# Performance work log

Measured on AMD Instinct MI355X. Metric: run time of the kernel, lower is better.

Reference implementation:

```python
import jax, jax.numpy as jnp
import numpy as np

K = 16  # kNN neighbors (global k in the original source)
# channel progression of the 6 DynamicEdgeConv layers
DIMS = [3, 32, 128, 256, 64, 32, 16]


def _knn_idx(x, k):
    # x: [B, N, D] -> indices of k nearest neighbors (incl. self), [B, N, k]
    sq = jnp.sum(x * x, axis=-1)                                   # [B, N]
    d = sq[:, :, None] + sq[:, None, :] - 2.0 * jnp.einsum('bnd,bmd->bnm', x, x)
    _, idx = jax.lax.top_k(-d, k)                                  # smallest distances
    return idx


def _edge_conv(x, W1, b1, W2, b2, k):
    # DynamicEdgeConv with mean aggregation: message = MLP([x_i, x_j - x_i])
    idx = _knn_idx(x, k)                                           # [B, N, k]
    xj = jax.vmap(lambda xb, ib: xb[ib])(x, idx)                   # [B, N, k, D]
    xi = jnp.broadcast_to(x[:, :, None, :], xj.shape)
    e = jnp.concatenate([xi, xj - xi], axis=-1)                    # [B, N, k, 2D]
    h = jax.nn.relu(e @ W1 + b1)
    h = jax.nn.relu(h @ W2 + b2)
    return jnp.mean(h, axis=2)                                     # [B, N, d_out]


def setup_inputs() -> dict:
    key = jax.random.key(0)
    ks = jax.random.split(key, 32)
    inp = {'x': jax.random.normal(ks[0], (8, 2048, 3), dtype=jnp.float32)}
    for l in range(6):
        din, dout = DIMS[l], DIMS[l + 1]
        s1 = 1.0 / np.sqrt(2 * din)
        s2 = 1.0 / np.sqrt(2 * dout)
        inp[f'W1_{l}'] = jax.random.normal(ks[1 + 4 * l], (2 * din, 2 * dout), dtype=jnp.float32) * s1
        inp[f'b1_{l}'] = jnp.zeros((2 * dout,), dtype=jnp.float32)
        inp[f'W2_{l}'] = jax.random.normal(ks[2 + 4 * l], (2 * dout, dout), dtype=jnp.float32) * s2
        inp[f'b2_{l}'] = jnp.zeros((dout,), dtype=jnp.float32)
    inp['Wf'] = jax.random.normal(ks[30], (16, 2), dtype=jnp.float32) * 0.25
    inp['bf'] = jnp.zeros((2,), dtype=jnp.float32)
    return inp


def reference(x, W1_0, b1_0, W2_0, b2_0, W1_1, b1_1, W2_1, b2_1,
              W1_2, b1_2, W2_2, b2_2, W1_3, b1_3, W2_3, b2_3,
              W1_4, b1_4, W2_4, b2_4, W1_5, b1_5, W2_5, b2_5, Wf, bf):
    params = [(W1_0, b1_0, W2_0, b2_0), (W1_1, b1_1, W2_1, b2_1),
              (W1_2, b1_2, W2_2, b2_2), (W1_3, b1_3, W2_3, b2_3),
              (W1_4, b1_4, W2_4, b2_4), (W1_5, b1_5, W2_5, b2_5)]
    for (W1, b1, W2, b2) in params:
        x = _edge_conv(x, W1, b1, W2, b2, K)
        x = jax.nn.relu(x)  # extra ReLU from forward (dropout is eval-mode identity)
    pooled = jnp.mean(x, axis=1)        # global_mean_pool over nodes -> [B, 16]
    return pooled @ Wf + bf             # [B, 2]
```

## Files before the change

kernel.cpp:

```cpp
#include <hip/hip_runtime.h>
#include <math.h>

#define NPTS 2048
#define NB 8
#define BN 16384
#define KNN 16

typedef _Float16 half4 __attribute__((ext_vector_type(4)));
typedef _Float16 half8 __attribute__((ext_vector_type(8)));
typedef float floatx16 __attribute__((ext_vector_type(16)));

__global__ __launch_bounds__(256) void sqprep_kernel(const float* __restrict__ X,
                                                     float* __restrict__ SQ,
                                                     const float* __restrict__ W1,
                                                     const float* __restrict__ b1,
                                                     float* __restrict__ Wcat,
                                                     float* __restrict__ bcat,
                                                     int din, int d2,
                                                     const float* __restrict__ W2,
                                                     _Float16* __restrict__ W2H,
                                                     _Float16* __restrict__ W2L,
                                                     int dout, int pb) {
    const int bid = blockIdx.x;
    if (bid < BN / 256) {
        int g = bid * 256 + threadIdx.x;
        const float* row = X + (size_t)g * din;
        float s = 0.f;
        for (int d = 0; d < din; ++d) s = fmaf(row[d], row[d], s);
        SQ[g] = s;
    } else if (bid < BN / 256 + pb) {
        int n4 = 2 * d2;
        int total = din * n4;
        int i = (bid - BN / 256) * 256 + threadIdx.x;
        if (i < total) {
            int d = i / n4, c = i - d * n4;
            float v;
            if (c < d2) v = W1[d * d2 + c] - W1[(din + d) * d2 + c];
            else        v = W1[(din + d) * d2 + (c - d2)];
            Wcat[i] = v;
        }
        if (i < n4) bcat[i] = (i < d2) ? b1[i] : 0.f;
    } else {
        int i = (bid - BN / 256 - pb) * 256 + threadIdx.x;
        if (i < d2 * dout) {
            int k = i / dout, c = i - k * dout;
            float wv = W2[i];
            _Float16 hv = (_Float16)wv;
            float rv = wv - (float)hv;
            W2H[(size_t)c * d2 + k] = hv;
            W2L[(size_t)c * d2 + k] = (_Float16)rv;
        }
    }
}

template <int DIN>
__global__ __launch_bounds__(256) void gram_kernel(const float* __restrict__ X,
                                                   const float* __restrict__ SQ,
                                                   float* __restrict__ DT) {
    __shared__ float As[32][132];
    __shared__ float Bs[32][132];
    const int t = threadIdx.x;
    const int tx = t & 15, ty = t >> 4;
    int bid = blockIdx.x;
    int bi = 0;
    while (bid >= 16 - bi) { bid -= 16 - bi; ++bi; }
    const int bj = bi + bid;
    const int i0 = bi * 128;
    const int j0 = bj * 128;
    const int z = blockIdx.z;
    const float* Xb = X + (size_t)z * NPTS * DIN;
    const float* SQb = SQ + (size_t)z * NPTS;
    float* DTb = DT + (size_t)z * NPTS * NPTS;

    const int e = t & 127;

    float acc[8][8];
    #pragma unroll
    for (int i = 0; i < 8; ++i)
        #pragma unroll
        for (int j = 0; j < 8; ++j) acc[i][j] = 0.f;

    if constexpr (DIN % 32 == 0) {
        const int rh = (t >> 7) * 16;
        const float* Ar = Xb + (size_t)(i0 + e) * DIN;
        const float* Br = Xb + (size_t)(j0 + e) * DIN;
        for (int k0 = 0; k0 < DIN; k0 += 32) {
            #pragma unroll
            for (int h = 0; h < 4; ++h) {
                float4 a = *(const float4*)(Ar + k0 + rh + h * 4);
                float4 b = *(const float4*)(Br + k0 + rh + h * 4);
                As[rh + h * 4 + 0][e] = a.x; As[rh + h * 4 + 1][e] = a.y;
                As[rh + h * 4 + 2][e] = a.z; As[rh + h * 4 + 3][e] = a.w;
                Bs[rh + h * 4 + 0][e] = b.x; Bs[rh + h * 4 + 1][e] = b.y;
                Bs[rh + h * 4 + 2][e] = b.z; Bs[rh + h * 4 + 3][e] = b.w;
            }
            __syncthreads();
            #pragma unroll
            for (int r = 0; r < 32; ++r) {
                float4 a0 = *(const float4*)&As[r][ty * 4];
                float4 a1 = *(const float4*)&As[r][64 + ty * 4];
                float4 b0 = *(const float4*)&Bs[r][tx * 4];
                float4 b1 = *(const float4*)&Bs[r][64 + tx * 4];
                float av[8] = {a0.x, a0.y, a0.z, a0.w, a1.x, a1.y, a1.z, a1.w};
                float bv[8] = {b0.x, b0.y, b0.z, b0.w, b1.x, b1.y, b1.z, b1.w};
                #pragma unroll
                for (int i = 0; i < 8; ++i)
                    #pragma unroll
                    for (int j = 0; j < 8; ++j)
                        acc[i][j] = fmaf(av[i], bv[j], acc[i][j]);
            }
            __syncthreads();
        }
    } else {
        const int rh = (t >> 7) * 8;
        #pragma unroll
        for (int i = 0; i < 8; ++i) {
            int k = rh + i;
            As[rh + i][e] = (k < DIN) ? Xb[(size_t)(i0 + e) * DIN + k] : 0.f;
            Bs[rh + i][e] = (k < DIN) ? Xb[(size_t)(j0 + e) * DIN + k] : 0.f;
        }
        __syncthreads();
        #pragma unroll
        for (int r = 0; r < 16; ++r) {
            float4 a0 = *(const float4*)&As[r][ty * 4];
            float4 a1 = *(const float4*)&As[r][64 + ty * 4];
            float4 b0 = *(const float4*)&Bs[r][tx * 4];
            float4 b1 = *(const float4*)&Bs[r][64 + tx * 4];
            float av[8] = {a0.x, a0.y, a0.z, a0.w, a1.x, a1.y, a1.z, a1.w};
            float bv[8] = {b0.x, b0.y, b0.z, b0.w, b1.x, b1.y, b1.z, b1.w};
            #pragma unroll
            for (int i = 0; i < 8; ++i)
                #pragma unroll
                for (int j = 0; j < 8; ++j)
                    acc[i][j] = fmaf(av[i], bv[j], acc[i][j]);
        }
        __syncthreads();
    }

    float sqi[8], sqj[8];
    #pragma unroll
    for (int i = 0; i < 8; ++i) {
        int ro = (i < 4) ? (ty * 4 + i) : (64 + ty * 4 + (i - 4));
        sqi[i] = SQb[i0 + ro];
    }
    #pragma unroll
    for (int j = 0; j < 8; ++j) {
        int co = (j < 4) ? (tx * 4 + j) : (64 + tx * 4 + (j - 4));
        sqj[j] = SQb[j0 + co];
    }
    #pragma unroll
    for (int i = 0; i < 8; ++i) {
        int ro = (i < 4) ? (ty * 4 + i) : (64 + ty * 4 + (i - 4));
        float* out = DTb + (size_t)(i0 + ro) * NPTS + j0;
        float4 o0, o1;
        o0.x = (sqi[i] + sqj[0]) - 2.f * acc[i][0];
        o0.y = (sqi[i] + sqj[1]) - 2.f * acc[i][1];
        o0.z = (sqi[i] + sqj[2]) - 2.f * acc[i][2];
        o0.w = (sqi[i] + sqj[3]) - 2.f * acc[i][3];
        o1.x = (sqi[i] + sqj[4]) - 2.f * acc[i][4];
        o1.y = (sqi[i] + sqj[5]) - 2.f * acc[i][5];
        o1.z = (sqi[i] + sqj[6]) - 2.f * acc[i][6];
        o1.w = (sqi[i] + sqj[7]) - 2.f * acc[i][7];
        *(float4*)(out + tx * 4) = o0;
        *(float4*)(out + 64 + tx * 4) = o1;
    }
    if (bi != bj) {
        #pragma unroll
        for (int j = 0; j < 8; ++j) {
            int co = (j < 4) ? (tx * 4 + j) : (64 + tx * 4 + (j - 4));
            float* out = DTb + (size_t)(j0 + co) * NPTS + i0;
            float4 o0, o1;
            o0.x = (sqi[0] + sqj[j]) - 2.f * acc[0][j];
            o0.y = (sqi[1] + sqj[j]) - 2.f * acc[1][j];
            o0.z = (sqi[2] + sqj[j]) - 2.f * acc[2][j];
            o0.w = (sqi[3] + sqj[j]) - 2.f * acc[3][j];
            o1.x = (sqi[4] + sqj[j]) - 2.f * acc[4][j];
            o1.y = (sqi[5] + sqj[j]) - 2.f * acc[5][j];
            o1.z = (sqi[6] + sqj[j]) - 2.f * acc[6][j];
            o1.w = (sqi[7] + sqj[j]) - 2.f * acc[7][j];
            *(float4*)(out + ty * 4) = o0;
            *(float4*)(out + 64 + ty * 4) = o1;
        }
    }
}

__global__ __launch_bounds__(256) void knn_select_kernel(const float* __restrict__ DT,
                                                         int* __restrict__ IDX, int qoff) {
    const int t = threadIdx.x;
    const int w = t >> 6, lane = t & 63;
    const int q = blockIdx.x * 4 + w;
    const float* dq = DT + (size_t)q * NPTS;
    const int l4 = lane << 2;

    float vals[32];
    #pragma unroll
    for (int s = 0; s < 8; ++s) {
        float4 v = *(const float4*)(dq + s * 256 + l4);
        vals[s * 4 + 0] = v.x; vals[s * 4 + 1] = v.y;
        vals[s * 4 + 2] = v.z; vals[s * 4 + 3] = v.w;
    }
    unsigned rm = 0;
    float best = INFINITY; int bslot = 32;
    #pragma unroll
    for (int sl = 0; sl < 32; ++sl)
        if (vals[sl] < best) { best = vals[sl]; bslot = sl; }

    for (int rep = 0; rep < KNN; ++rep) {
        int bj = (bslot < 32) ? ((bslot >> 2) * 256 + l4 + (bslot & 3)) : NPTS;
        float gb = best; int gj = bj;
        #pragma unroll
        for (int off = 1; off < 64; off <<= 1) {
            float ov = __shfl_xor(gb, off);
            int oj = __shfl_xor(gj, off);
            if (ov < gb || (ov == gb && oj < gj)) { gb = ov; gj = oj; }
        }
        if (lane == 0) IDX[(size_t)(qoff + q) * KNN + rep] = gj;
        if (((gj >> 2) & 63) == lane) {
            int slot = ((gj >> 8) << 2) | (gj & 3);
            rm |= (1u << slot);
            best = INFINITY; bslot = 32;
            #pragma unroll
            for (int sl = 0; sl < 32; ++sl)
                if (!(rm & (1u << sl)) && vals[sl] < best) { best = vals[sl]; bslot = sl; }
        }
    }
}

template <int KK, int NN>
__global__ __launch_bounds__(256) void gemm_big_kernel(const float* __restrict__ A,
                                                       const float* __restrict__ B,
                                                       const float* __restrict__ bias,
                                                       float* __restrict__ C) {
    __shared__ float As[32][132];
    __shared__ float Bs[32][132];
    const int t = threadIdx.x;
    const int tx = t & 15, ty = t >> 4;
    const int m0 = blockIdx.x * 128;
    const int c0 = blockIdx.y * 128;

    float acc[8][8];
    #pragma unroll
    for (int i = 0; i < 8; ++i)
        #pragma unroll
        for (int j = 0; j < 8; ++j) acc[i][j] = 0.f;

    const int e = t & 127;
    const int rh = (t >> 7) * 16;
    const float* Ar = A + (size_t)(m0 + e) * KK + rh;
    const int br = t & 31;
    const int bc = (t >> 5) * 16;
    const float* Wbase = B + (size_t)br * NN + c0 + bc;

    for (int k0 = 0; k0 < KK; k0 += 32) {
        #pragma unroll
        for (int h = 0; h < 4; ++h) {
            float4 a = *(const float4*)(Ar + k0 + h * 4);
            As[rh + h * 4 + 0][e] = a.x; As[rh + h * 4 + 1][e] = a.y;
            As[rh + h * 4 + 2][e] = a.z; As[rh + h * 4 + 3][e] = a.w;
            *(float4*)&Bs[br][bc + h * 4] = *(const float4*)(Wbase + (size_t)k0 * NN + h * 4);
        }
        __syncthreads();
        #pragma unroll
        for (int r = 0; r < 32; ++r) {
            float4 a0 = *(const float4*)&As[r][ty * 4];
            float4 a1 = *(const float4*)&As[r][64 + ty * 4];
            float4 b0 = *(const float4*)&Bs[r][tx * 4];
            float4 b1 = *(const float4*)&Bs[r][64 + tx * 4];
            float av[8] = {a0.x, a0.y, a0.z, a0.w, a1.x, a1.y, a1.z, a1.w};
            float bv[8] = {b0.x, b0.y, b0.z, b0.w, b1.x, b1.y, b1.z, b1.w};
            #pragma unroll
            for (int i = 0; i < 8; ++i)
                #pragma unroll
                for (int j = 0; j < 8; ++j)
                    acc[i][j] = fmaf(av[i], bv[j], acc[i][j]);
        }
        __syncthreads();
    }

    float bvv[8];
    #pragma unroll
    for (int j = 0; j < 8; ++j) {
        int co = (j < 4) ? (tx * 4 + j) : (64 + tx * 4 + (j - 4));
        bvv[j] = bias[c0 + co];
    }
    #pragma unroll
    for (int i = 0; i < 8; ++i) {
        int ro = (i < 4) ? (ty * 4 + i) : (64 + ty * 4 + (i - 4));
        float* out = C + (size_t)(m0 + ro) * NN + c0;
        float4 o0, o1;
        o0.x = acc[i][0] + bvv[0]; o0.y = acc[i][1] + bvv[1];
        o0.z = acc[i][2] + bvv[2]; o0.w = acc[i][3] + bvv[3];
        o1.x = acc[i][4] + bvv[4]; o1.y = acc[i][5] + bvv[5];
        o1.z = acc[i][6] + bvv[6]; o1.w = acc[i][7] + bvv[7];
        *(float4*)(out + tx * 4) = o0;
        *(float4*)(out + 64 + tx * 4) = o1;
    }
}

template <int KK, int NN>
__global__ __launch_bounds__(256) void gemm_pq_kernel(const float* __restrict__ A,
                                                      const float* __restrict__ B,
                                                      const float* __restrict__ bias,
                                                      float* __restrict__ C) {
    __shared__ float As[16][68];
    __shared__ float Bs[16][64];
    const int t = threadIdx.x;
    const int tx = t & 15, ty = t >> 4;
    const int m0 = blockIdx.x * 64;
    const int c0 = blockIdx.y * 64;
    float acc[4][4];
    #pragma unroll
    for (int i = 0; i < 4; ++i)
        #pragma unroll
        for (int j = 0; j < 4; ++j) acc[i][j] = 0.f;

    constexpr int KCH = (KK + 15) / 16;
    for (int kc = 0; kc < KCH; ++kc) {
        const int k0 = kc * 16;
        {
            int m = t & 63;
            int r4 = (t >> 6) * 4;
            if constexpr (KK % 16 == 0) {
                float4 v = *(const float4*)(A + (size_t)(m0 + m) * KK + k0 + r4);
                As[r4 + 0][m] = v.x; As[r4 + 1][m] = v.y;
                As[r4 + 2][m] = v.z; As[r4 + 3][m] = v.w;
            } else {
                #pragma unroll
                for (int i = 0; i < 4; ++i) {
                    int r = r4 + i;
                    As[r][m] = (k0 + r < KK) ? A[(size_t)(m0 + m) * KK + k0 + r] : 0.f;
                }
            }
        }
        {
            int r = t >> 4;
            int c = (t & 15) * 4;
            float4 v = make_float4(0.f, 0.f, 0.f, 0.f);
            if (k0 + r < KK) v = *(const float4*)(B + (size_t)(k0 + r) * NN + c0 + c);
            *(float4*)&Bs[r][c] = v;
        }
        __syncthreads();
        #pragma unroll
        for (int r = 0; r < 16; ++r) {
            float4 a4 = *(const float4*)&As[r][ty * 4];
            float4 b4 = *(const float4*)&Bs[r][tx * 4];
            float av[4] = {a4.x, a4.y, a4.z, a4.w};
            float bv[4] = {b4.x, b4.y, b4.z, b4.w};
            #pragma unroll
            for (int i = 0; i < 4; ++i)
                #pragma unroll
                for (int j = 0; j < 4; ++j)
                    acc[i][j] = fmaf(av[i], bv[j], acc[i][j]);
        }
        __syncthreads();
    }
    float4 bv4 = *(const float4*)(bias + c0 + tx * 4);
    float bv[4] = {bv4.x, bv4.y, bv4.z, bv4.w};
    #pragma unroll
    for (int i = 0; i < 4; ++i) {
        float4 o;
        o.x = acc[i][0] + bv[0];
        o.y = acc[i][1] + bv[1];
        o.z = acc[i][2] + bv[2];
        o.w = acc[i][3] + bv[3];
        *(float4*)(C + (size_t)(m0 + ty * 4 + i) * NN + c0 + tx * 4) = o;
    }
}

template <int D2, int DOUT>
__global__ __launch_bounds__(256) void edge_kernel(const float* __restrict__ PQ,
                                                   const int* __restrict__ IDX,
                                                   const float* __restrict__ W2,
                                                   const float* __restrict__ b2,
                                                   float* __restrict__ Xn) {
    constexpr int N4 = 2 * D2;
    __shared__ float As[16][68];
    __shared__ float Bs[16][64];
    __shared__ int gjs[64];
    const int t = threadIdx.x;
    const int tx = t & 15, ty = t >> 4;
    const int nb = blockIdx.x * 4;
    const int c0 = blockIdx.y * 64;

    if (t < 64) {
        int node = nb + (t >> 4);
        int bstart = (node / NPTS) * NPTS;
        gjs[t] = bstart + IDX[(size_t)node * KNN + (t & 15)];
    }
    __syncthreads();

    float acc[4][4];
    #pragma unroll
    for (int i = 0; i < 4; ++i)
        #pragma unroll
        for (int j = 0; j < 4; ++j) acc[i][j] = 0.f;

    const int e = t & 63;
    const int r4 = (t >> 6) * 4;
    const int gi = nb + (e >> 4);

    for (int k0 = 0; k0 < D2; k0 += 16) {
        {
            int gj = gjs[e];
            float4 p = *(const float4*)(PQ + (size_t)gi * N4 + k0 + r4);
            float4 q = *(const float4*)(PQ + (size_t)gj * N4 + D2 + k0 + r4);
            As[r4 + 0][e] = fmaxf(p.x + q.x, 0.f);
            As[r4 + 1][e] = fmaxf(p.y + q.y, 0.f);
            As[r4 + 2][e] = fmaxf(p.z + q.z, 0.f);
            As[r4 + 3][e] = fmaxf(p.w + q.w, 0.f);
        }
        {
            int r = t >> 4;
            int c = (t & 15) * 4;
            float4 v = make_float4(0.f, 0.f, 0.f, 0.f);
            if (c0 + c < DOUT) v = *(const float4*)(W2 + (size_t)(k0 + r) * DOUT + c0 + c);
            *(float4*)&Bs[r][c] = v;
        }
        __syncthreads();
        #pragma unroll
        for (int r = 0; r < 16; ++r) {
            float4 a4 = *(const float4*)&As[r][ty * 4];
            float4 b4 = *(const float4*)&Bs[r][tx * 4];
            float av[4] = {a4.x, a4.y, a4.z, a4.w};
            float bv[4] = {b4.x, b4.y, b4.z, b4.w};
            #pragma unroll
            for (int i = 0; i < 4; ++i)
                #pragma unroll
                for (int j = 0; j < 4; ++j)
                    acc[i][j] = fmaf(av[i], bv[j], acc[i][j]);
        }
        __syncthreads();
    }

    float bv[4];
    #pragma unroll
    for (int j = 0; j < 4; ++j) {
        int c = c0 + tx * 4 + j;
        bv[j] = (c < DOUT) ? b2[c] : 0.f;
    }
    float s[4];
    #pragma unroll
    for (int j = 0; j < 4; ++j) {
        float ss = 0.f;
        #pragma unroll
        for (int i = 0; i < 4; ++i) ss += fmaxf(acc[i][j] + bv[j], 0.f);
        s[j] = ss;
    }
    #pragma unroll
    for (int j = 0; j < 4; ++j) Bs[ty][tx * 4 + j] = s[j];
    __syncthreads();
    if ((ty & 3) == 0) {
        int node = nb + (ty >> 2);
        #pragma unroll
        for (int j = 0; j < 4; ++j) {
            int c = c0 + tx * 4 + j;
            if (c < DOUT) {
                int cc = tx * 4 + j;
                float tot = Bs[ty][cc] + Bs[ty + 1][cc] + Bs[ty + 2][cc] + Bs[ty + 3][cc];
                Xn[(size_t)node * DOUT + c] = tot * (1.f / 16.f);
            }
        }
    }
}

#define EB_STAGE_MFMA(KC, QQ, POK, KP)                                               \
  {                                                                                  \
    half8 wh0 = *(const half8*)(WHrow + (KC) + rh);                                  \
    half8 wh1 = *(const half8*)(WHrow + (KC) + rh + 8);                              \
    half8 wl0 = *(const half8*)(WLrow + (KC) + rh);                                  \
    half8 wl1 = *(const half8*)(WLrow + (KC) + rh + 8);                              \
    _Pragma("unroll")                                                                \
    for (int h = 0; h < 4; ++h) {                                                    \
      float4 p = *(const float4*)(Prow + (KC) + rh + h * 4);                         \
      float a0 = fmaxf(p.x + QQ[h].x, 0.f);                                          \
      float a1 = fmaxf(p.y + QQ[h].y, 0.f);                                          \
      float a2 = fmaxf(p.z + QQ[h].z, 0.f);                                          \
      float a3 = fmaxf(p.w + QQ[h].w, 0.f);                                          \
      _Float16 h0 = (_Float16)a0, h1 = (_Float16)a1;                                 \
      _Float16 h2 = (_Float16)a2, h3 = (_Float16)a3;                                 \
      half4 hv, lv;                                                                  \
      hv.x = h0; hv.y = h1; hv.z = h2; hv.w = h3;                                    \
      lv.x = (_Float16)(a0 - (float)h0);                                             \
      lv.y = (_Float16)(a1 - (float)h1);                                             \
      lv.z = (_Float16)(a2 - (float)h2);                                             \
      lv.w = (_Float16)(a3 - (float)h3);                                             \
      *(half4*)&Ah[e][rh + h * 4] = hv;                                              \
      *(half4*)&Al[e][rh + h * 4] = lv;                                              \
    }                                                                                \
    *(half8*)&Bh[e][rh] = wh0;                                                       \
    *(half8*)&Bh[e][rh + 8] = wh1;                                                   \
    *(half8*)&Bl[e][rh] = wl0;                                                       \
    *(half8*)&Bl[e][rh + 8] = wl1;                                                   \
    if (POK) {                                                                       \
      _Pragma("unroll")                                                              \
      for (int h = 0; h < 4; ++h)                                                    \
        QQ[h] = *(const float4*)(Qrow + (KP) + rh + h * 4);                          \
    }                                                                                \
    asm volatile("s_waitcnt lgkmcnt(0)" ::: "memory");                               \
    __builtin_amdgcn_s_barrier();                                                    \
    asm volatile("" ::: "memory");                                                   \
    _Pragma("unroll")                                                                \
    for (int ks = 0; ks < 2; ++ks) {                                                 \
      const int kb = ks * 16 + lk;                                                   \
      half8 bf0 = *(const half8*)&Bh[wc + lr][kb];                                   \
      half8 blf0 = *(const half8*)&Bl[wc + lr][kb];                                  \
      half8 bf1 = *(const half8*)&Bh[wc + 32 + lr][kb];                              \
      half8 blf1 = *(const half8*)&Bl[wc + 32 + lr][kb];                             \
      _Pragma("unroll")                                                              \
      for (int i = 0; i < 2; ++i) {                                                  \
        half8 af = *(const half8*)&Ah[wr + i * 32 + lr][kb];                         \
        half8 alf = *(const half8*)&Al[wr + i * 32 + lr][kb];                        \
        acc[i][0] = __builtin_amdgcn_mfma_f32_32x32x16_f16(af, bf0, acc[i][0], 0, 0, 0);   \
        acc[i][0] = __builtin_amdgcn_mfma_f32_32x32x16_f16(af, blf0, acc[i][0], 0, 0, 0);  \
        acc[i][0] = __builtin_amdgcn_mfma_f32_32x32x16_f16(alf, bf0, acc[i][0], 0, 0, 0);  \
        acc[i][1] = __builtin_amdgcn_mfma_f32_32x32x16_f16(af, bf1, acc[i][1], 0, 0, 0);   \
        acc[i][1] = __builtin_amdgcn_mfma_f32_32x32x16_f16(af, blf1, acc[i][1], 0, 0, 0);  \
        acc[i][1] = __builtin_amdgcn_mfma_f32_32x32x16_f16(alf, bf1, acc[i][1], 0, 0, 0);  \
      }                                                                              \
    }                                                                                \
    asm volatile("" ::: "memory");                                                   \
    __builtin_amdgcn_s_barrier();                                                    \
    asm volatile("" ::: "memory");                                                   \
  }

template <int D2, int DOUT>
__global__ __launch_bounds__(256) void edge_big_mfma_kernel(const float* __restrict__ PQ,
                                                            const int* __restrict__ IDX,
                                                            const _Float16* __restrict__ W2H,
                                                            const _Float16* __restrict__ W2L,
                                                            const float* __restrict__ b2,
                                                            float* __restrict__ Xn) {
    constexpr int N4 = 2 * D2;
    __shared__ _Float16 Ah[128][40];
    __shared__ _Float16 Al[128][40];
    __shared__ _Float16 Bh[128][40];
    __shared__ _Float16 Bl[128][40];
    __shared__ int gjs[128];
    const int t = threadIdx.x;
    const int nb8 = blockIdx.x * 8;
    const int c0 = blockIdx.y * 128;

    if (t < 128) {
        int node = nb8 + (t >> 4);
        int bstart = (node / NPTS) * NPTS;
        gjs[t] = bstart + IDX[(size_t)node * KNN + (t & 15)];
    }
    __syncthreads();

    const int e = t & 127;
    const int rh = (t >> 7) * 16;
    const int gi = nb8 + (e >> 4);
    const int gj = gjs[e];
    const float* Prow = PQ + (size_t)gi * N4;
    const float* Qrow = PQ + (size_t)gj * N4 + D2;
    const _Float16* WHrow = W2H + (size_t)(c0 + e) * D2;
    const _Float16* WLrow = W2L + (size_t)(c0 + e) * D2;

    const int w = t >> 6;
    const int lane = t & 63;
    const int wr = (w >> 1) * 64;
    const int wc = (w & 1) * 64;
    const int lr = lane & 31;
    const int lk = (lane >> 5) * 8;
    const int hsel = lane >> 5;

    floatx16 acc[2][2];
    #pragma unroll
    for (int i = 0; i < 2; ++i)
        #pragma unroll
        for (int j = 0; j < 2; ++j)
            #pragma unroll
            for (int r = 0; r < 16; ++r) acc[i][j][r] = 0.f;

    float4 qqA[4], qqB[4];
    #pragma unroll
    for (int h = 0; h < 4; ++h) qqA[h] = *(const float4*)(Qrow + rh + h * 4);
    #pragma unroll
    for (int h = 0; h < 4; ++h) qqB[h] = *(const float4*)(Qrow + 32 + rh + h * 4);

    for (int k0 = 0; k0 < D2; k0 += 64) {
        EB_STAGE_MFMA(k0,      qqA, (k0 + 64 < D2), k0 + 64)
        EB_STAGE_MFMA(k0 + 32, qqB, (k0 + 96 < D2), k0 + 96)
    }

    float bb[2];
    bb[0] = b2[c0 + wc + lr];
    bb[1] = b2[c0 + wc + 32 + lr];
    #pragma unroll
    for (int i = 0; i < 2; ++i) {
        int node0 = nb8 + ((wr + i * 32) >> 4);
        #pragma unroll
        for (int j = 0; j < 2; ++j) {
            float sA = 0.f, sB = 0.f;
            #pragma unroll
            for (int r = 0; r < 8; ++r)  sA += fmaxf(acc[i][j][r] + bb[j], 0.f);
            #pragma unroll
            for (int r = 8; r < 16; ++r) sB += fmaxf(acc[i][j][r] + bb[j], 0.f);
            sA += __shfl_xor(sA, 32);
            sB += __shfl_xor(sB, 32);
            if (hsel == 0) {
                int col = c0 + wc + j * 32 + lr;
                Xn[(size_t)node0 * DOUT + col] = sA * (1.f / 16.f);
                Xn[(size_t)(node0 + 1) * DOUT + col] = sB * (1.f / 16.f);
            }
        }
    }
}
#undef EB_STAGE_MFMA

#define EM_STAGE_MFMA(KC, QQ, POK, KP)                                               \
  {                                                                                  \
    half8 wh0 = *(const half8*)(WHrow + (KC));                                       \
    half8 wl0 = *(const half8*)(WLrow + (KC));                                       \
    _Pragma("unroll")                                                                \
    for (int h = 0; h < 4; ++h) {                                                    \
      float4 p = *(const float4*)(Prow + (KC) + rh + h * 4);                         \
      float a0 = fmaxf(p.x + QQ[h].x, 0.f);                                          \
      float a1 = fmaxf(p.y + QQ[h].y, 0.f);                                          \
      float a2 = fmaxf(p.z + QQ[h].z, 0.f);                                          \
      float a3 = fmaxf(p.w + QQ[h].w, 0.f);                                          \
      _Float16 h0 = (_Float16)a0, h1 = (_Float16)a1;                                 \
      _Float16 h2 = (_Float16)a2, h3 = (_Float16)a3;                                 \
      half4 hv, lv;                                                                  \
      hv.x = h0; hv.y = h1; hv.z = h2; hv.w = h3;                                    \
      lv.x = (_Float16)(a0 - (float)h0);                                             \
      lv.y = (_Float16)(a1 - (float)h1);                                             \
      lv.z = (_Float16)(a2 - (float)h2);                                             \
      lv.w = (_Float16)(a3 - (float)h3);                                             \
      *(half4*)&Ah[e][rh + h * 4] = hv;                                              \
      *(half4*)&Al[e][rh + h * 4] = lv;                                              \
    }                                                                                \
    *(half8*)&Bh[wrB][wkB] = wh0;                                                    \
    *(half8*)&Bl[wrB][wkB] = wl0;                                                    \
    if (POK) {                                                                       \
      _Pragma("unroll")                                                              \
      for (int h = 0; h < 4; ++h)                                                    \
        QQ[h] = *(const float4*)(Qrow + (KP) + rh + h * 4);                          \
    }                                                                                \
    asm volatile("s_waitcnt lgkmcnt(0)" ::: "memory");                               \
    __builtin_amdgcn_s_barrier();                                                    \
    asm volatile("" ::: "memory");                                                   \
    _Pragma("unroll")                                                                \
    for (int ks = 0; ks < 2; ++ks) {                                                 \
      const int kb = ks * 16 + lk;                                                   \
      half8 bf0 = *(const half8*)&Bh[wc + lr][kb];                                   \
      half8 blf0 = *(const half8*)&Bl[wc + lr][kb];                                  \
      _Pragma("unroll")                                                              \
      for (int i = 0; i < 2; ++i) {                                                  \
        half8 af = *(const half8*)&Ah[wr + i * 32 + lr][kb];                         \
        half8 alf = *(const half8*)&Al[wr + i * 32 + lr][kb];                        \
        acc[i] = __builtin_amdgcn_mfma_f32_32x32x16_f16(af, bf0, acc[i], 0, 0, 0);   \
        acc[i] = __builtin_amdgcn_mfma_f32_32x32x16_f16(af, blf0, acc[i], 0, 0, 0);  \
        acc[i] = __builtin_amdgcn_mfma_f32_32x32x16_f16(alf, bf0, acc[i], 0, 0, 0);  \
      }                                                                              \
    }                                                                                \
    asm volatile("" ::: "memory");                                                   \
    __builtin_amdgcn_s_barrier();                                                    \
    asm volatile("" ::: "memory");                                                   \
  }

template <int D2, int DOUT>
__global__ __launch_bounds__(256) void edge_mid_mfma_kernel(const float* __restrict__ PQ,
                                                            const int* __restrict__ IDX,
                                                            const _Float16* __restrict__ W2H,
                                                            const _Float16* __restrict__ W2L,
                                                            const float* __restrict__ b2,
                                                            float* __restrict__ Xn) {
    constexpr int N4 = 2 * D2;
    __shared__ _Float16 Ah[128][40];
    __shared__ _Float16 Al[128][40];
    __shared__ _Float16 Bh[64][40];
    __shared__ _Float16 Bl[64][40];
    __shared__ int gjs[128];
    const int t = threadIdx.x;
    const int nb8 = blockIdx.x * 8;

    if (t < 128) {
        int node = nb8 + (t >> 4);
        int bstart = (node / NPTS) * NPTS;
        gjs[t] = bstart + IDX[(size_t)node * KNN + (t & 15)];
    }
    __syncthreads();

    const int e = t & 127;
    const int rh = (t >> 7) * 16;
    const int gi = nb8 + (e >> 4);
    const int gj = gjs[e];
    const float* Prow = PQ + (size_t)gi * N4;
    const float* Qrow = PQ + (size_t)gj * N4 + D2;
    const int wrB = t & 63;
    const int wkB = (t >> 6) * 8;
    const _Float16* WHrow = W2H + (size_t)wrB * D2 + wkB;
    const _Float16* WLrow = W2L + (size_t)wrB * D2 + wkB;

    const int w = t >> 6;
    const int lane = t & 63;
    const int wr = (w >> 1) * 64;
    const int wc = (w & 1) * 32;
    const int lr = lane & 31;
    const int lk = (lane >> 5) * 8;
    const int hsel = lane >> 5;

    floatx16 acc[2];
    #pragma unroll
    for (int i = 0; i < 2; ++i)
        #pragma unroll
        for (int r = 0; r < 16; ++r) acc[i][r] = 0.f;

    float4 qqA[4], qqB[4];
    #pragma unroll
    for (int h = 0; h < 4; ++h) qqA[h] = *(const float4*)(Qrow + rh + h * 4);
    #pragma unroll
    for (int h = 0; h < 4; ++h) qqB[h] = *(const float4*)(Qrow + 32 + rh + h * 4);

    for (int k0 = 0; k0 < D2; k0 += 64) {
        EM_STAGE_MFMA(k0,      qqA, (k0 + 64 < D2), k0 + 64)
        EM_STAGE_MFMA(k0 + 32, qqB, (k0 + 96 < D2), k0 + 96)
    }

    float bb = b2[wc + lr];
    #pragma unroll
    for (int i = 0; i < 2; ++i) {
        int node0 = nb8 + ((wr + i * 32) >> 4);
        float sA = 0.f, sB = 0.f;
        #pragma unroll
        for (int r = 0; r < 8; ++r)  sA += fmaxf(acc[i][r] + bb, 0.f);
        #pragma unroll
        for (int r = 8; r < 16; ++r) sB += fmaxf(acc[i][r] + bb, 0.f);
        sA += __shfl_xor(sA, 32);
        sB += __shfl_xor(sB, 32);
        if (hsel == 0) {
            int col = wc + lr;
            Xn[(size_t)node0 * DOUT + col] = sA * (1.f / 16.f);
            Xn[(size_t)(node0 + 1) * DOUT + col] = sB * (1.f / 16.f);
        }
    }
}
#undef EM_STAGE_MFMA

__global__ __launch_bounds__(256) void final_kernel(const float* __restrict__ X,
                                                    const float* __restrict__ Wf,
                                                    const float* __restrict__ bfin,
                                                    float* __restrict__ out) {
    __shared__ float red[16][17];
    __shared__ float pool[16];
    const int b = blockIdx.x;
    const int t = threadIdx.x;
    const int c = t & 15, rg = t >> 4;
    float s = 0.f;
    for (int n = rg; n < NPTS; n += 16) s += X[(size_t)(b * NPTS + n) * 16 + c];
    red[rg][c] = s;
    __syncthreads();
    if (t < 16) {
        float tot = 0.f;
        #pragma unroll
        for (int i = 0; i < 16; ++i) tot += red[i][t];
        pool[t] = tot * (1.f / NPTS);
    }
    __syncthreads();
    if (t < 2) {
        float a = bfin[t];
        #pragma unroll
        for (int cc = 0; cc < 16; ++cc) a = fmaf(pool[cc], Wf[cc * 2 + t], a);
        out[b * 2 + t] = a;
    }
}

template <int DIN, int DOUT>
static void run_layer(const float* Xin, float* Xout, float* PQ, float* SQ, int* IDX,
                      float* WCAT, float* BCAT, _Float16* W2H, _Float16* W2L,
                      const float* W1, const float* b1, const float* W2, const float* b2,
                      hipStream_t stream) {
    constexpr int D2 = 2 * DOUT;
    constexpr int N4 = 2 * D2;
    constexpr int prep_blocks = (DIN * N4 + 255) / 256;
    constexpr int w2_blocks = (DOUT >= 64) ? ((D2 * DOUT + 255) / 256) : 0;
    sqprep_kernel<<<BN / 256 + prep_blocks + w2_blocks, 256, 0, stream>>>(
        Xin, SQ, W1, b1, WCAT, BCAT, DIN, D2, W2, W2H, W2L,
        (DOUT >= 64) ? DOUT : 0, prep_blocks);
    for (int h = 0; h < 2; ++h) {
        dim3 gg(136, 1, 4);
        gram_kernel<DIN><<<gg, 256, 0, stream>>>(Xin + (size_t)h * 4 * NPTS * DIN,
                                                 SQ + (size_t)h * 4 * NPTS, PQ);
        knn_select_kernel<<<2048, 256, 0, stream>>>(PQ, IDX, h * 8192);
    }
    if constexpr (N4 % 128 == 0 && DIN % 32 == 0) {
        dim3 g1(BN / 128, N4 / 128);
        gemm_big_kernel<DIN, N4><<<g1, 256, 0, stream>>>(Xin, WCAT, BCAT, PQ);
    } else {
        dim3 g1(BN / 64, N4 / 64);
        gemm_pq_kernel<DIN, N4><<<g1, 256, 0, stream>>>(Xin, WCAT, BCAT, PQ);
    }
    if constexpr (DOUT >= 128) {
        dim3 g2(BN / 8, DOUT / 128);
        edge_big_mfma_kernel<D2, DOUT><<<g2, 256, 0, stream>>>(PQ, IDX, W2H, W2L, b2, Xout);
    } else if constexpr (DOUT == 64) {
        dim3 g2(BN / 8, 1);
        edge_mid_mfma_kernel<D2, DOUT><<<g2, 256, 0, stream>>>(PQ, IDX, W2H, W2L, b2, Xout);
    } else {
        dim3 g2(BN / 4, (DOUT + 63) / 64);
        edge_kernel<D2, DOUT><<<g2, 256, 0, stream>>>(PQ, IDX, W2, b2, Xout);
    }
}

extern "C" void kernel_launch(void* const* d_in, const int* in_sizes, int n_in,
                              void* d_out, int out_size, void* d_ws, size_t ws_size,
                              hipStream_t stream) {
    (void)in_sizes; (void)n_in; (void)out_size; (void)ws_size;
    const float* x = (const float*)d_in[0];
    const float* W1a[6]; const float* b1a[6]; const float* W2a[6]; const float* b2a[6];
    for (int l = 0; l < 6; ++l) {
        W1a[l] = (const float*)d_in[1 + 4 * l];
        b1a[l] = (const float*)d_in[2 + 4 * l];
        W2a[l] = (const float*)d_in[3 + 4 * l];
        b2a[l] = (const float*)d_in[4 + 4 * l];
    }
    const float* Wf = (const float*)d_in[25];
    const float* bfin = (const float*)d_in[26];

    float* ws = (float*)d_ws;
    float* X0   = ws;
    float* X1   = X0 + (size_t)BN * 256;
    float* PQ   = X1 + (size_t)BN * 256;
    float* SQ   = PQ + (size_t)BN * 1024;
    int*   IDX  = (int*)(SQ + BN);
    float* WCAT = (float*)(IDX + (size_t)BN * KNN);
    float* BCAT = WCAT + 131072;
    _Float16* W2H = (_Float16*)(BCAT + 1024);
    _Float16* W2L = W2H + 131072;

    run_layer<3,   32>(x,  X0, PQ, SQ, IDX, WCAT, BCAT, W2H, W2L, W1a[0], b1a[0], W2a[0], b2a[0], stream);
    run_layer<32, 128>(X0, X1, PQ, SQ, IDX, WCAT, BCAT, W2H, W2L, W1a[1], b1a[1], W2a[1], b2a[1], stream);
    run_layer<128,256>(X1, X0, PQ, SQ, IDX, WCAT, BCAT, W2H, W2L, W1a[2], b1a[2], W2a[2], b2a[2], stream);
    run_layer<256, 64>(X0, X1, PQ, SQ, IDX, WCAT, BCAT, W2H, W2L, W1a[3], b1a[3], W2a[3], b2a[3], stream);
    run_layer<64,  32>(X1, X0, PQ, SQ, IDX, WCAT, BCAT, W2H, W2L, W1a[4], b1a[4], W2a[4], b2a[4], stream);
    run_layer<32,  16>(X0, X1, PQ, SQ, IDX, WCAT, BCAT, W2H, W2L, W1a[5], b1a[5], W2a[5], b2a[5], stream);
    final_kernel<<<NB, 256, 0, stream>>>(X1, Wf, bfin, (float*)d_out);
}
```

Baseline: 1.849 ms.

## Double-buffer LDS and double the edge tile in big MFMA edge kernel

After: 1.845 ms. Within noise of the previous version (-0.2%).

```diff
diff --git a/kernel.cpp b/kernel.cpp
--- a/kernel.cpp
+++ b/kernel.cpp
@@ -463,19 +463,22 @@
     }
 }
 
-#define EB_STAGE_MFMA(KC, QQ, POK, KP)                                               \
-  {                                                                                  \
-    half8 wh0 = *(const half8*)(WHrow + (KC) + rh);                                  \
-    half8 wh1 = *(const half8*)(WHrow + (KC) + rh + 8);                              \
-    half8 wl0 = *(const half8*)(WLrow + (KC) + rh);                                  \
-    half8 wl1 = *(const half8*)(WLrow + (KC) + rh + 8);                              \
-    _Pragma("unroll")                                                                \
+#define EBG_LOAD(KN)                                                                 \
+  { _Pragma("unroll")                                                                \
     for (int h = 0; h < 4; ++h) {                                                    \
-      float4 p = *(const float4*)(Prow + (KC) + rh + h * 4);                         \
-      float a0 = fmaxf(p.x + QQ[h].x, 0.f);                                          \
-      float a1 = fmaxf(p.y + QQ[h].y, 0.f);                                          \
-      float a2 = fmaxf(p.z + QQ[h].z, 0.f);                                          \
-      float a3 = fmaxf(p.w + QQ[h].w, 0.f);                                          \
+      pp[h] = *(const float4*)(Prow + (KN) + rh + h * 4);                            \
+      qq[h] = *(const float4*)(Qrow + (KN) + rh + h * 4);                            \
+    }                                                                                \
+    wh = *(const half8*)(WHrow + (KN));                                              \
+    wl = *(const half8*)(WLrow + (KN)); }
+
+#define EBG_STAGE(dst)                                                               \
+  { _Pragma("unroll")                                                                \
+    for (int h = 0; h < 4; ++h) {                                                    \
+      float a0 = fmaxf(pp[h].x + qq[h].x, 0.f);                                      \
+      float a1 = fmaxf(pp[h].y + qq[h].y, 0.f);                                      \
+      float a2 = fmaxf(pp[h].z + qq[h].z, 0.f);                                      \
+      float a3 = fmaxf(pp[h].w + qq[h].w, 0.f);                                      \
       _Float16 h0 = (_Float16)a0, h1 = (_Float16)a1;                                 \
       _Float16 h2 = (_Float16)a2, h3 = (_Float16)a3;                                 \
       half4 hv, lv;                                                                  \
@@ -484,77 +487,68 @@
       lv.y = (_Float16)(a1 - (float)h1);                                             \
       lv.z = (_Float16)(a2 - (float)h2);                                             \
       lv.w = (_Float16)(a3 - (float)h3);                                             \
-      *(half4*)&Ah[e][rh + h * 4] = hv;                                              \
-      *(half4*)&Al[e][rh + h * 4] = lv;                                              \
+      *(half4*)&Ah[dst][e][rh + h * 4] = hv;                                         \
+      *(half4*)&Al[dst][e][rh + h * 4] = lv;                                         \
     }                                                                                \
-    *(half8*)&Bh[e][rh] = wh0;                                                       \
-    *(half8*)&Bh[e][rh + 8] = wh1;                                                   \
-    *(half8*)&Bl[e][rh] = wl0;                                                       \
-    *(half8*)&Bl[e][rh + 8] = wl1;                                                   \
-    if (POK) {                                                                       \
-      _Pragma("unroll")                                                              \
-      for (int h = 0; h < 4; ++h)                                                    \
-        QQ[h] = *(const float4*)(Qrow + (KP) + rh + h * 4);                          \
-    }                                                                                \
-    asm volatile("s_waitcnt lgkmcnt(0)" ::: "memory");                               \
-    __builtin_amdgcn_s_barrier();                                                    \
-    asm volatile("" ::: "memory");                                                   \
-    _Pragma("unroll")                                                                \
+    *(half8*)&Bh[dst][eb][rb] = wh;                                                  \
+    *(half8*)&Bl[dst][eb][rb] = wl; }
+
+#define EBG_MFMA(cur)                                                                \
+  { _Pragma("unroll")                                                                \
     for (int ks = 0; ks < 2; ++ks) {                                                 \
       const int kb = ks * 16 + lk;                                                   \
-      half8 bf0 = *(const half8*)&Bh[wc + lr][kb];                                   \
-      half8 blf0 = *(const half8*)&Bl[wc + lr][kb];                                  \
-      half8 bf1 = *(const half8*)&Bh[wc + 32 + lr][kb];                              \
-      half8 blf1 = *(const half8*)&Bl[wc + 32 + lr][kb];                             \
+      half8 bf0  = *(const half8*)&Bh[cur][wc + lr][kb];                             \
+      half8 blf0 = *(const half8*)&Bl[cur][wc + lr][kb];                             \
+      half8 bf1  = *(const half8*)&Bh[cur][wc + 32 + lr][kb];                        \
+      half8 blf1 = *(const half8*)&Bl[cur][wc + 32 + lr][kb];                        \
       _Pragma("unroll")                                                              \
       for (int i = 0; i < 2; ++i) {                                                  \
-        half8 af = *(const half8*)&Ah[wr + i * 32 + lr][kb];                         \
-        half8 alf = *(const half8*)&Al[wr + i * 32 + lr][kb];                        \
-        acc[i][0] = __builtin_amdgcn_mfma_f32_32x32x16_f16(af, bf0, acc[i][0], 0, 0, 0);   \
-        acc[i][0] = __builtin_amdgcn_mfma_f32_32x32x16_f16(af, blf0, acc[i][0], 0, 0, 0);  \
-        acc[i][0] = __builtin_amdgcn_mfma_f32_32x32x16_f16(alf, bf0, acc[i][0], 0, 0, 0);  \
-        acc[i][1] = __builtin_amdgcn_mfma_f32_32x32x16_f16(af, bf1, acc[i][1], 0, 0, 0);   \
-        acc[i][1] = __builtin_amdgcn_mfma_f32_32x32x16_f16(af, blf1, acc[i][1], 0, 0, 0);  \
-        acc[i][1] = __builtin_amdgcn_mfma_f32_32x32x16_f16(alf, bf1, acc[i][1], 0, 0, 0);  \
+        half8 af  = *(const half8*)&Ah[cur][wr + i * 32 + lr][kb];                   \
+        half8 alf = *(const half8*)&Al[cur][wr + i * 32 + lr][kb];                   \
+        acc[i][0] = __builtin_amdgcn_mfma_f32_32x32x16_f16(af,  bf0,  acc[i][0], 0, 0, 0); \
+        acc[i][0] = __builtin_amdgcn_mfma_f32_32x32x16_f16(af,  blf0, acc[i][0], 0, 0, 0); \
+        acc[i][0] = __builtin_amdgcn_mfma_f32_32x32x16_f16(alf, bf0,  acc[i][0], 0, 0, 0); \
+        acc[i][1] = __builtin_amdgcn_mfma_f32_32x32x16_f16(af,  bf1,  acc[i][1], 0, 0, 0); \
+        acc[i][1] = __builtin_amdgcn_mfma_f32_32x32x16_f16(af,  blf1, acc[i][1], 0, 0, 0); \
+        acc[i][1] = __builtin_amdgcn_mfma_f32_32x32x16_f16(alf, bf1,  acc[i][1], 0, 0, 0); \
       }                                                                              \
-    }                                                                                \
-    asm volatile("" ::: "memory");                                                   \
-    __builtin_amdgcn_s_barrier();                                                    \
-    asm volatile("" ::: "memory");                                                   \
-  }
+    } }
 
 template <int D2, int DOUT>
-__global__ __launch_bounds__(256) void edge_big_mfma_kernel(const float* __restrict__ PQ,
+__global__ __launch_bounds__(512) void edge_big_mfma_kernel(const float* __restrict__ PQ,
                                                             const int* __restrict__ IDX,
                                                             const _Float16* __restrict__ W2H,
                                                             const _Float16* __restrict__ W2L,
                                                             const float* __restrict__ b2,
                                                             float* __restrict__ Xn) {
     constexpr int N4 = 2 * D2;
-    __shared__ _Float16 Ah[128][40];
-    __shared__ _Float16 Al[128][40];
-    __shared__ _Float16 Bh[128][40];
-    __shared__ _Float16 Bl[128][40];
-    __shared__ int gjs[128];
+    constexpr int NSTEP = D2 / 32;
+    __shared__ _Float16 Ah[2][256][40];
+    __shared__ _Float16 Al[2][256][40];
+    __shared__ _Float16 Bh[2][128][40];
+    __shared__ _Float16 Bl[2][128][40];
+    __shared__ int gjs[256];
     const int t = threadIdx.x;
-    const int nb8 = blockIdx.x * 8;
+    const int nb16 = blockIdx.x * 16;
     const int c0 = blockIdx.y * 128;
 
-    if (t < 128) {
-        int node = nb8 + (t >> 4);
+    if (t < 256) {
+        int node = nb16 + (t >> 4);
         int bstart = (node / NPTS) * NPTS;
         gjs[t] = bstart + IDX[(size_t)node * KNN + (t & 15)];
     }
     __syncthreads();
 
-    const int e = t & 127;
-    const int rh = (t >> 7) * 16;
-    const int gi = nb8 + (e >> 4);
+    const int e  = t & 255;
+    const int rh = (t >> 8) * 16;
+    const int gi = nb16 + (e >> 4);
     const int gj = gjs[e];
     const float* Prow = PQ + (size_t)gi * N4;
     const float* Qrow = PQ + (size_t)gj * N4 + D2;
-    const _Float16* WHrow = W2H + (size_t)(c0 + e) * D2;
-    const _Float16* WLrow = W2L + (size_t)(c0 + e) * D2;
+    const int eb = t & 127;
+    const int rb = (t >> 7) * 8;
+    const _Float16* WHrow = W2H + (size_t)(c0 + eb) * D2 + rb;
+    const _Float16* WLrow = W2L + (size_t)(c0 + eb) * D2 + rb;
 
     const int w = t >> 6;
     const int lane = t & 63;
@@ -572,23 +566,34 @@
             #pragma unroll
             for (int r = 0; r < 16; ++r) acc[i][j][r] = 0.f;
 
-    float4 qqA[4], qqB[4];
-    #pragma unroll
-    for (int h = 0; h < 4; ++h) qqA[h] = *(const float4*)(Qrow + rh + h * 4);
-    #pragma unroll
-    for (int h = 0; h < 4; ++h) qqB[h] = *(const float4*)(Qrow + 32 + rh + h * 4);
-
-    for (int k0 = 0; k0 < D2; k0 += 64) {
-        EB_STAGE_MFMA(k0,      qqA, (k0 + 64 < D2), k0 + 64)
-        EB_STAGE_MFMA(k0 + 32, qqB, (k0 + 96 < D2), k0 + 96)
-    }
+    float4 pp[4], qq[4];
+    half8 wh, wl;
+
+    EBG_LOAD(0)
+    EBG_STAGE(0)
+    EBG_LOAD(32)
+    asm volatile("s_waitcnt lgkmcnt(0)" ::: "memory");
+    __builtin_amdgcn_s_barrier();
+    asm volatile("" ::: "memory");
+
+    for (int s = 0; s < NSTEP - 1; ++s) {
+        const int cur = s & 1;
+        EBG_MFMA(cur)
+        EBG_STAGE(cur ^ 1)
+        const int kn = (s + 2 < NSTEP) ? (s + 2) * 32 : (NSTEP - 1) * 32;
+        EBG_LOAD(kn)
+        asm volatile("s_waitcnt lgkmcnt(0)" ::: "memory");
+        __builtin_amdgcn_s_barrier();
+        asm volatile("" ::: "memory");
+    }
+    EBG_MFMA((NSTEP - 1) & 1)
 
     float bb[2];
     bb[0] = b2[c0 + wc + lr];
     bb[1] = b2[c0 + wc + 32 + lr];
     #pragma unroll
     for (int i = 0; i < 2; ++i) {
-        int node0 = nb8 + ((wr + i * 32) >> 4);
+        int node0 = nb16 + ((wr + i * 32) >> 4);
         #pragma unroll
         for (int j = 0; j < 2; ++j) {
             float sA = 0.f, sB = 0.f;
@@ -606,7 +611,9 @@
         }
     }
 }
-#undef EB_STAGE_MFMA
+#undef EBG_LOAD
+#undef EBG_STAGE
+#undef EBG_MFMA
 
 #define EM_STAGE_MFMA(KC, QQ, POK, KP)                                               \
   {                                                                                  \
@@ -792,8 +799,8 @@
         gemm_pq_kernel<DIN, N4><<<g1, 256, 0, stream>>>(Xin, WCAT, BCAT, PQ);
     }
     if constexpr (DOUT >= 128) {
-        dim3 g2(BN / 8, DOUT / 128);
-        edge_big_mfma_kernel<D2, DOUT><<<g2, 256, 0, stream>>>(PQ, IDX, W2H, W2L, b2, Xout);
+        dim3 g2(BN / 16, DOUT / 128);
+        edge_big_mfma_kernel<D2, DOUT><<<g2, 512, 0, stream>>>(PQ, IDX, W2H, W2L, b2, Xout);
     } else if constexpr (DOUT == 64) {
         dim3 g2(BN / 8, 1);
         edge_mid_mfma_kernel<D2, DOUT><<<g2, 256, 0, stream>>>(PQ, IDX, W2H, W2L, b2, Xout);
```
